# Kernel tuning notes

Hardware: AMD Instinct MI355X
Metric: run time of the kernel (lower is better)

Reference implementation:

```python
import jax, jax.numpy as jnp
import numpy as np
from jax import lax

B, C, H, W = 64, 512, 14, 14
HEAD_DIM = 32
NUM_HEADS = C // HEAD_DIM
HIDDEN = int(C * 4.0)
EPS = 1e-5
LS_INIT = 1e-5


def setup_inputs() -> dict:
    key = jax.random.key(0)
    ks = jax.random.split(key, 16)
    d = {}
    d['x'] = jax.random.normal(ks[0], (B, C, H, W), dtype=jnp.float32)
    # shared BatchNorm2d(dim) (inference-mode, running stats)
    d['bn_g'] = 1.0 + 0.1 * jax.random.normal(ks[1], (C,), dtype=jnp.float32)
    d['bn_b'] = 0.1 * jax.random.normal(ks[2], (C,), dtype=jnp.float32)
    d['bn_m'] = 0.1 * jax.random.normal(ks[3], (C,), dtype=jnp.float32)
    d['bn_v'] = jax.random.uniform(ks[4], (C,), minval=0.5, maxval=1.5, dtype=jnp.float32)
    # MHSA params (qkv_bias=False)
    d['qkv_w'] = 0.02 * jax.random.normal(ks[5], (3 * C, C), dtype=jnp.float32)
    d['proj_w'] = 0.02 * jax.random.normal(ks[6], (C, C), dtype=jnp.float32)
    d['proj_b'] = jnp.zeros((C,), dtype=jnp.float32)
    # ConvFFN: depthwise 7x7 (groups=C, no bias) -> BN -> 1x1 -> GELU -> 1x1
    d['dw_w'] = 0.02 * jax.random.normal(ks[7], (C, 1, 7, 7), dtype=jnp.float32)
    d['fbn_g'] = 1.0 + 0.1 * jax.random.normal(ks[8], (C,), dtype=jnp.float32)
    d['fbn_b'] = 0.1 * jax.random.normal(ks[9], (C,), dtype=jnp.float32)
    d['fbn_m'] = 0.1 * jax.random.normal(ks[10], (C,), dtype=jnp.float32)
    d['fbn_v'] = jax.random.uniform(ks[11], (C,), minval=0.5, maxval=1.5, dtype=jnp.float32)
    d['fc1_w'] = 0.02 * jax.random.normal(ks[12], (HIDDEN, C), dtype=jnp.float32)
    d['fc1_b'] = jnp.zeros((HIDDEN,), dtype=jnp.float32)
    d['fc2_w'] = 0.02 * jax.random.normal(ks[13], (C, HIDDEN), dtype=jnp.float32)
    d['fc2_b'] = jnp.zeros((C,), dtype=jnp.float32)
    # layer scale params, shape (C,1,1)
    d['ls1'] = LS_INIT * jnp.ones((C, 1, 1), dtype=jnp.float32)
    d['ls2'] = LS_INIT * jnp.ones((C, 1, 1), dtype=jnp.float32)
    return d


def _bn2d(x, g, b, m, v):
    # inference BatchNorm2d over channel dim of NCHW
    inv = g * lax.rsqrt(v + EPS)
    return x * inv[None, :, None, None] + (b - m * inv)[None, :, None, None]


def _mhsa(x, qkv_w, proj_w, proj_b):
    b, c, h, w = x.shape
    n = h * w
    xt = x.reshape(b, c, n).transpose(0, 2, 1)              # [B,N,C]
    qkv = xt @ qkv_w.T                                       # [B,N,3C]
    qkv = qkv.reshape(b, n, 3, NUM_HEADS, HEAD_DIM).transpose(2, 0, 3, 1, 4)
    q, k, v = qkv[0], qkv[1], qkv[2]                         # [B,h,N,d]
    scale = HEAD_DIM ** -0.5
    attn = jax.nn.softmax(jnp.einsum('bhnd,bhmd->bhnm', q * scale, k), axis=-1)
    o = jnp.einsum('bhnm,bhmd->bhnd', attn, v)               # [B,h,N,d]
    o = o.transpose(0, 2, 1, 3).reshape(b, n, c)             # [B,N,C]
    o = o @ proj_w.T + proj_b
    return o.transpose(0, 2, 1).reshape(b, c, h, w)


def _convffn(x, dw_w, fbn_g, fbn_b, fbn_m, fbn_v, fc1_w, fc1_b, fc2_w, fc2_b):
    y = lax.conv_general_dilated(x, dw_w, window_strides=(1, 1),
                                 padding=[(3, 3), (3, 3)],
                                 feature_group_count=C,
                                 dimension_numbers=('NCHW', 'OIHW', 'NCHW'))
    y = _bn2d(y, fbn_g, fbn_b, fbn_m, fbn_v)
    y = jnp.einsum('bchw,oc->bohw', y, fc1_w) + fc1_b[None, :, None, None]
    y = jax.nn.gelu(y, approximate=False)
    y = jnp.einsum('bchw,oc->bohw', y, fc2_w) + fc2_b[None, :, None, None]
    return y


def reference(x, bn_g, bn_b, bn_m, bn_v, qkv_w, proj_w, proj_b,
              dw_w, fbn_g, fbn_b, fbn_m, fbn_v, fc1_w, fc1_b, fc2_w, fc2_b,
              ls1, ls2):
    xn = _bn2d(x, bn_g, bn_b, bn_m, bn_v)
    x = x + ls1[None] * _mhsa(xn, qkv_w, proj_w, proj_b)
    xn = _bn2d(x, bn_g, bn_b, bn_m, bn_v)
    x = x + ls2[None] * _convffn(xn, dw_w, fbn_g, fbn_b, fbn_m, fbn_v,
                                 fc1_w, fc1_b, fc2_w, fc2_b)
    return x
```

## Files before the change

kernel.cpp:

```cpp
#include <hip/hip_runtime.h>
#include <hip/hip_bf16.h>
#include <hip/hip_fp8.h>
#include <stdint.h>

#define NTOK 196
#define NB   64
#define CCH  512
#define HID  2048
#define MTOT (NB * NTOK)

typedef __attribute__((ext_vector_type(8))) short  short8v;
typedef __attribute__((ext_vector_type(4))) float  float4v;
typedef __attribute__((ext_vector_type(2))) int    int2v;


__device__ __forceinline__ void mfma_fp8(float4v& d, int2v a, int2v b) {
  asm("v_mfma_f32_16x16x32_fp8_fp8 %0, %1, %2, %0" : "+v"(d) : "v"(a), "v"(b));
}

__device__ __forceinline__ void gload_lds16(const void* gsrc, void* ldst) {
  __builtin_amdgcn_global_load_lds(
      (const __attribute__((address_space(1))) unsigned int*)gsrc,
      (__attribute__((address_space(3))) unsigned int*)ldst, 16, 0, 0);
}

__device__ __forceinline__ int swz4(int r) { return (r ^ (r >> 2)) & 3; }

__device__ __forceinline__ uint32_t cvt2_fp8(float a, float b) {
  uint32_t d;
  asm("v_cvt_pk_fp8_f32 %0, %1, %2" : "=v"(d) : "v"(a), "v"(b));
  return d;
}


__global__ void prep_consts(const float* __restrict__ bn_g, const float* __restrict__ bn_b,
                            const float* __restrict__ bn_m, const float* __restrict__ bn_v,
                            const float* __restrict__ fbn_g, const float* __restrict__ fbn_b,
                            const float* __restrict__ fbn_m, const float* __restrict__ fbn_v,
                            float* __restrict__ cst) {
  int c = blockIdx.x * blockDim.x + threadIdx.x;
  if (c < CCH) {
    float i1 = bn_g[c] * rsqrtf(bn_v[c] + 1e-5f);
    cst[c] = i1;
    cst[512 + c] = bn_b[c] - bn_m[c] * i1;
    float i2 = fbn_g[c] * rsqrtf(fbn_v[c] + 1e-5f);
    cst[1024 + c] = i2;
    cst[1536 + c] = fbn_b[c] - fbn_m[c] * i2;
  }
}


__global__ void cvt_weights(const float* __restrict__ qkv_w, const float* __restrict__ proj_w,
                            const float* __restrict__ fc1_w, const float* __restrict__ fc2_w,
                            uint8_t* __restrict__ qkvb, uint8_t* __restrict__ projb,
                            uint8_t* __restrict__ fc1b, uint8_t* __restrict__ fc2b) {
  int i4 = blockIdx.x * blockDim.x + threadIdx.x;
  const int nq = 1536 * 512 / 4;
  const int np = 512 * 512 / 4;
  const int n1 = 2048 * 512 / 4;
  const float* src;
  uint8_t* dst;
  int k;
  if (i4 < nq)                { src = qkv_w;  dst = qkvb;  k = i4; }
  else if (i4 < nq + np)      { src = proj_w; dst = projb; k = i4 - nq; }
  else if (i4 < nq + np + n1) { src = fc1_w;  dst = fc1b;  k = i4 - nq - np; }
  else                        { src = fc2_w;  dst = fc2b;  k = i4 - nq - np - n1; }
  float4v v = *(const float4v*)(src + 4 * (size_t)k);
  uint32_t w0 = cvt2_fp8(v[0] * 16.0f, v[1] * 16.0f);
  uint32_t w1 = cvt2_fp8(v[2] * 16.0f, v[3] * 16.0f);
  *(uint16_t*)(dst + 4 * (size_t)k)     = (uint16_t)w0;
  *(uint16_t*)(dst + 4 * (size_t)k + 2) = (uint16_t)w1;
}


__global__ __launch_bounds__(256) void transpose_x(
    const float* __restrict__ x, uint8_t* __restrict__ xnt8,
    __hip_bfloat16* __restrict__ xt, const float* __restrict__ cst) {
  __shared__ float tile[32][33];
  const int n0 = blockIdx.x * 32;
  const int c0 = blockIdx.y * 32;
  const int b  = blockIdx.z;
  const int j = threadIdx.x & 31, i = threadIdx.x >> 5;
  #pragma unroll
  for (int p = 0; p < 4; ++p) {
    int cc = c0 + i + p * 8;
    int n = n0 + j;
    if (n < NTOK) tile[i + p * 8][j] = x[((size_t)b * CCH + cc) * NTOK + n];
  }
  __syncthreads();
  const float s = cst[c0 + j], t = cst[512 + c0 + j];
  float bn[4];
  size_t off[4];
  bool ok[4];
  #pragma unroll
  for (int p = 0; p < 4; ++p) {
    int n = n0 + i + p * 8;
    int cc = c0 + j;
    ok[p] = (n < NTOK);
    if (ok[p]) {
      float raw = tile[j][i + p * 8];
      size_t o = ((size_t)b * NTOK + n) * CCH + cc;
      xt[o] = __float2bfloat16(raw);
      bn[p] = raw * s + t;
      off[p] = o;
    }
  }
  uint32_t w0 = cvt2_fp8(bn[0], bn[1]);
  uint32_t w1 = cvt2_fp8(bn[2], bn[3]);
  if (ok[0]) xnt8[off[0]] = (uint8_t)w0;
  if (ok[1]) xnt8[off[1]] = (uint8_t)(w0 >> 8);
  if (ok[2]) xnt8[off[2]] = (uint8_t)w1;
  if (ok[3]) xnt8[off[3]] = (uint8_t)(w1 >> 8);
}


template<int EPI>
__global__ __launch_bounds__(256, 3) void gemm8f(
    const uint8_t* __restrict__ A, const uint8_t* __restrict__ Bw,
    int N, int K, int NY,
    __hip_bfloat16* __restrict__ outb, uint8_t* __restrict__ out8,
    float* __restrict__ outf,
    const float* __restrict__ bias, const float* __restrict__ ls,
    const __hip_bfloat16* __restrict__ resid) {
  __shared__ char lds[49152];
  const int tid  = threadIdx.x;
  const int lane = tid & 63;
  const int wave = tid >> 6;

  const int q    = (int)gridDim.x >> 3;
  const int orig = blockIdx.x;
  const int wgid = (orig & 7) * q + (orig >> 3);
  const int bx = wgid / NY;
  const int by = wgid - bx * NY;

  const int m0 = bx * 128;
  const int n0 = by * 128;
  const int wm = (wave >> 1) * 64;
  const int wn = (wave & 1) * 64;
  const int KT = K >> 6;

  float4v acc[4][4] = {};

  auto stage = [&](int buf, int kt) {
    const int kb = kt * 64;
    char* base = lds + buf * 16384;
    #pragma unroll
    for (int i = 0; i < 2; ++i) {
      int L = i * 4096 + tid * 16;
      int row = L >> 6;
      int lc = ((L >> 4) & 3) ^ swz4(row);
      gload_lds16(A + (size_t)(m0 + row) * K + kb + lc * 16, base + L);
    }
    #pragma unroll
    for (int i = 0; i < 2; ++i) {
      int L = i * 4096 + tid * 16;
      int row = L >> 6;
      int lc = ((L >> 4) & 3) ^ swz4(row);
      gload_lds16(Bw + (size_t)(n0 + row) * K + kb + lc * 16, base + 8192 + L);
    }
  };

  auto compute = [&](int buf) {
    const char* bA = lds + buf * 16384;
    const char* bB = bA + 8192;
    const int g = lane >> 4;
    #pragma unroll
    for (int t = 0; t < 2; ++t) {
      int2v av[4], bv[4];
      #pragma unroll
      for (int f = 0; f < 4; ++f) {
        int row = wm + f * 16 + (lane & 15);
        int c16 = ((t << 1) | (g >> 1)) ^ swz4(row);
        av[f] = *(const int2v*)(bA + row * 64 + c16 * 16 + (g & 1) * 8);
      }
      #pragma unroll
      for (int j = 0; j < 4; ++j) {
        int row = wn + j * 16 + (lane & 15);
        int c16 = ((t << 1) | (g >> 1)) ^ swz4(row);
        bv[j] = *(const int2v*)(bB + row * 64 + c16 * 16 + (g & 1) * 8);
      }
      #pragma unroll
      for (int i = 0; i < 4; ++i)
        #pragma unroll
        for (int j = 0; j < 4; ++j)
          mfma_fp8(acc[i][j], av[i], bv[j]);
    }
  };

  stage(0, 0);
  stage(1, 1);
  int cur = 0;
  for (int kt = 0; kt < KT - 1; ++kt) {
    asm volatile("s_waitcnt vmcnt(4)" ::: "memory");
    __builtin_amdgcn_s_barrier();
    __builtin_amdgcn_sched_barrier(0);
    if (kt + 2 < KT) {
      int s = cur + 2; if (s >= 3) s -= 3;
      stage(s, kt + 2);
    }
    compute(cur);
    ++cur; if (cur == 3) cur = 0;
  }
  asm volatile("s_waitcnt vmcnt(0)" ::: "memory");
  __builtin_amdgcn_s_barrier();
  __builtin_amdgcn_sched_barrier(0);
  compute(cur);
  asm volatile("s_nop 7\n\ts_nop 7");

  const float RS = 0.0625f;

  if (EPI == 0) {
    #pragma unroll
    for (int i = 0; i < 4; ++i)
      #pragma unroll
      for (int j = 0; j < 4; ++j)
        #pragma unroll
        for (int r = 0; r < 4; r += 2) {
          int m = m0 + wm + i * 16 + ((lane >> 4) << 2) + r;
          int n = n0 + wn + j * 16 + (lane & 15);
          int bb = m / NTOK, tok = m - bb * NTOK;
          int bb2 = (m + 1) / NTOK, tok2 = (m + 1) - bb2 * NTOK;
          int sel = n >> 9, hh = (n >> 5) & 15, d = n & 31;
          uint32_t w = cvt2_fp8(acc[i][j][r] * RS, acc[i][j][r + 1] * RS);
          out8[(((size_t)(sel * 16 + hh) * NB + bb) * NTOK + tok) * 32 + d]  = (uint8_t)w;
          out8[(((size_t)(sel * 16 + hh) * NB + bb2) * NTOK + tok2) * 32 + d] = (uint8_t)(w >> 8);
        }
  } else if (EPI == 2) {
    #pragma unroll
    for (int i = 0; i < 4; ++i)
      #pragma unroll
      for (int j = 0; j < 4; ++j)
        #pragma unroll
        for (int r = 0; r < 4; r += 2) {
          int m = m0 + wm + i * 16 + ((lane >> 4) << 2) + r;
          int n = n0 + wn + j * 16 + (lane & 15);
          float z0 = acc[i][j][r] * RS + bias[n];
          float z1 = acc[i][j][r + 1] * RS + bias[n];
          float g0 = z0 / (1.0f + __expf(-1.702f * z0));
          float g1 = z1 / (1.0f + __expf(-1.702f * z1));
          uint32_t w = cvt2_fp8(g0, g1);
          out8[(size_t)m * N + n]       = (uint8_t)w;
          out8[(size_t)(m + 1) * N + n] = (uint8_t)(w >> 8);
        }
  } else if (EPI == 1) {
    #pragma unroll
    for (int i = 0; i < 4; ++i)
      #pragma unroll
      for (int j = 0; j < 4; ++j)
        #pragma unroll
        for (int r = 0; r < 4; ++r) {
          int m = m0 + wm + i * 16 + ((lane >> 4) << 2) + r;
          int n = n0 + wn + j * 16 + (lane & 15);
          float v = acc[i][j][r] * RS + bias[n];
          v = __bfloat162float(resid[(size_t)m * CCH + n]) + ls[n] * v;
          outb[(size_t)m * CCH + n] = __float2bfloat16(v);
        }
  } else {
    float* LT = (float*)lds;
    #pragma unroll 1
    for (int hh = 0; hh < 2; ++hh) {
      __syncthreads();
      if ((wn >> 6) == hh) {
        #pragma unroll
        for (int i = 0; i < 4; ++i)
          #pragma unroll
          for (int j = 0; j < 4; ++j)
            #pragma unroll
            for (int r = 0; r < 4; ++r) {
              int ml = wm + i * 16 + ((lane >> 4) << 2) + r;
              int nl = j * 16 + (lane & 15);
              int n = n0 + wn + nl;
              float v = acc[i][j][r] * RS + bias[n];
              v = __bfloat162float(resid[(size_t)(m0 + ml) * CCH + n]) + ls[n] * v;
              LT[nl * 129 + ml] = v;
            }
      }
      __syncthreads();
      {
        int ml0 = lane << 1;
        int mg = m0 + ml0;
        int bb0 = mg / NTOK;
        int tt0 = mg - bb0 * NTOK;
        int bb1 = (mg + 1) / NTOK;
        int tt1 = (mg + 1) - bb1 * NTOK;
        size_t base0 = (size_t)bb0 * (CCH * NTOK) + tt0;
        size_t base1 = (size_t)bb1 * (CCH * NTOK) + tt1;
        #pragma unroll
        for (int u = 0; u < 16; ++u) {
          int cr = wave * 16 + u;
          int cg = n0 + hh * 64 + cr;
          float v0 = LT[cr * 129 + ml0];
          float v1 = LT[cr * 129 + ml0 + 1];
          outf[base0 + (size_t)cg * NTOK] = v0;
          outf[base1 + (size_t)cg * NTOK] = v1;
        }
      }
    }
  }
}


__global__ __launch_bounds__(256, 3) void attn_kernel(
    const uint8_t* __restrict__ qkv8, uint8_t* __restrict__ o_t8) {
  __shared__ char sQ[208 * 48];
  __shared__ char sK[224 * 48];
  __shared__ char sV[32 * 240];
  __shared__ char sP[4][16 * 232];
  const int tid  = threadIdx.x;
  const int lane = tid & 63;
  const int wave = tid >> 6;
  const int b = blockIdx.x >> 4;
  const int h = blockIdx.x & 15;
  const size_t CHB = 6272;
  const uint8_t* Qg = qkv8 + ((size_t)(0 * 16 + h) * NB + b) * CHB;
  const uint8_t* Kg = qkv8 + ((size_t)(1 * 16 + h) * NB + b) * CHB;
  const uint8_t* Vg = qkv8 + ((size_t)(2 * 16 + h) * NB + b) * CHB;

  for (int i = tid; i < 144; i += 256) {
    int r = i / 12, w = i % 12;
    ((uint32_t*)(sQ + (196 + r) * 48))[w] = 0u;
  }
  for (int i = tid; i < 336; i += 256) {
    int r = i / 12, w = i % 12;
    ((uint32_t*)(sK + (196 + r) * 48))[w] = 0u;
  }
  for (int i = tid; i < 352; i += 256) {
    int d = i / 11, w = i % 11;
    ((uint32_t*)(sV + d * 240 + 196))[w] = 0u;
  }

  for (int c = tid; c < 392; c += 256) {
    int row = c >> 1, hf = c & 1;
    uint4 vq = *(const uint4*)(Qg + c * 16);
    *(uint4*)(sQ + row * 48 + hf * 16) = vq;
    uint4 vk = *(const uint4*)(Kg + c * 16);
    *(uint4*)(sK + row * 48 + hf * 16) = vk;
  }
  for (int u = tid; u < 784; u += 256) {
    int row = u >> 2, d0 = (u & 3) * 8;
    uint64_t w = *(const uint64_t*)(Vg + (size_t)u * 8);
    #pragma unroll
    for (int e = 0; e < 8; ++e)
      sV[(d0 + e) * 240 + row] = (char)(w >> (8 * e));
  }
  __syncthreads();

  const float scale = 0.17677669529663687f;
  char* Pw = sP[wave];
  const int g = lane >> 4;

  for (int mt = wave; mt < 13; mt += 4) {
    int qrow = mt * 16 + (lane & 15);
    int2v aq = *(const int2v*)(sQ + qrow * 48 + g * 8);

    float4v s[14];
    #pragma unroll
    for (int nt = 0; nt < 14; ++nt) {
      int krow = nt * 16 + (lane & 15);
      int2v bk = *(const int2v*)(sK + krow * 48 + g * 8);
      s[nt] = float4v{0.f, 0.f, 0.f, 0.f};
      mfma_fp8(s[nt], aq, bk);
    }
    asm volatile("s_nop 7\n\ts_nop 7");

    float mx[4] = {-INFINITY, -INFINITY, -INFINITY, -INFINITY};
    #pragma unroll
    for (int nt = 0; nt < 14; ++nt) {
      bool valid = (nt * 16 + (lane & 15)) < NTOK;
      #pragma unroll
      for (int r = 0; r < 4; ++r) {
        float v = valid ? s[nt][r] * scale : -INFINITY;
        s[nt][r] = v;
        mx[r] = fmaxf(mx[r], v);
      }
    }
    #pragma unroll
    for (int off = 1; off < 16; off <<= 1) {
      #pragma unroll
      for (int r = 0; r < 4; ++r) mx[r] = fmaxf(mx[r], __shfl_xor(mx[r], off));
    }
    float sum[4] = {0.f, 0.f, 0.f, 0.f};
    #pragma unroll
    for (int nt = 0; nt < 14; ++nt) {
      #pragma unroll
      for (int r = 0; r < 4; ++r) {
        float e = __expf(s[nt][r] - mx[r]);
        s[nt][r] = e;
        sum[r] += e;
      }
    }
    #pragma unroll
    for (int off = 1; off < 16; off <<= 1) {
      #pragma unroll
      for (int r = 0; r < 4; ++r) sum[r] += __shfl_xor(sum[r], off);
    }
    float rs[4];
    #pragma unroll
    for (int r = 0; r < 4; ++r) rs[r] = 1.0f / sum[r];

    #pragma unroll
    for (int nt = 0; nt < 14; ++nt) {
      int col = nt * 16 + (lane & 15);
      #pragma unroll
      for (int r = 0; r < 4; r += 2) {
        int prow = ((lane >> 4) << 2) + r;
        uint32_t w = cvt2_fp8(s[nt][r], s[nt][r + 1]);
        *(uint8_t*)(Pw + prow * 232 + col)       = (uint8_t)w;
        *(uint8_t*)(Pw + (prow + 1) * 232 + col) = (uint8_t)(w >> 8);
      }
    }

    float4v o0 = float4v{0.f, 0.f, 0.f, 0.f};
    float4v o1 = float4v{0.f, 0.f, 0.f, 0.f};
    #pragma unroll
    for (int ks = 0; ks < 7; ++ks) {
      int2v pa = *(const int2v*)(Pw + (lane & 15) * 232 + ks * 32 + g * 8);
      int2v v0 = *(const int2v*)(sV + (lane & 15) * 240 + ks * 32 + g * 8);
      int2v v1 = *(const int2v*)(sV + (16 + (lane & 15)) * 240 + ks * 32 + g * 8);
      mfma_fp8(o0, pa, v0);
      mfma_fp8(o1, pa, v1);
    }
    asm volatile("s_nop 7\n\ts_nop 7");

    #pragma unroll
    for (int r = 0; r < 4; ++r) {
      int trow = mt * 16 + ((lane >> 4) << 2) + r;
      if (trow < NTOK) {
        size_t ob = ((size_t)b * NTOK + trow) * CCH + h * 32 + (lane & 15);
        uint32_t w = cvt2_fp8(o0[r] * rs[r], o1[r] * rs[r]);
        o_t8[ob]      = (uint8_t)w;
        o_t8[ob + 16] = (uint8_t)(w >> 8);
      }
    }
  }
}


__global__ __launch_bounds__(448) void dwconv_tm(
    const __hip_bfloat16* __restrict__ x1t, const float* __restrict__ dw_w,
    const float* __restrict__ cst, uint8_t* __restrict__ yt8) {
  __shared__ float img[196][32];
  __shared__ float wgt[49][32];
  const int tid = threadIdx.x;
  const int b  = blockIdx.x >> 4;
  const int cb = (blockIdx.x & 15) * 32;
  const int c  = tid & 31;
  const int gc = cb + c;
  const float s = cst[gc], t0 = cst[512 + gc];
  #pragma unroll
  for (int k = 0; k < 14; ++k) {
    int p = (tid >> 5) + k * 14;
    img[p][c] = __bfloat162float(x1t[((size_t)b * NTOK + p) * CCH + gc]) * s + t0;
  }
  for (int i = tid; i < 49 * 32; i += 448) {
    int tap = i >> 5, cc = i & 31;
    wgt[tap][cc] = dw_w[(cb + cc) * 49 + tap];
  }
  __syncthreads();

  const int px = tid >> 5;
  float out[14];
  #pragma unroll
  for (int i = 0; i < 14; ++i) out[i] = 0.f;
  #pragma unroll 1
  for (int row = 0; row < 14; ++row) {
    float v[7];
    #pragma unroll
    for (int dx = 0; dx < 7; ++dx) {
      int ix = px + dx - 3;
      v[dx] = ((unsigned)ix < 14u) ? img[row * 14 + ix][c] : 0.f;
    }
    #pragma unroll
    for (int kk = 0; kk < 7; ++kk) {
      int py = row + 3 - kk;
      if (py >= 0 && py < 14) {
        float hsum = 0.f;
        #pragma unroll
        for (int dx = 0; dx < 7; ++dx) hsum = fmaf(v[dx], wgt[kk * 7 + dx][c], hsum);
        out[py] += hsum;
      }
    }
  }
  const float fs = cst[1024 + gc], ft = cst[1536 + gc];
  #pragma unroll
  for (int py = 0; py < 14; py += 2) {
    uint32_t w = cvt2_fp8(out[py] * fs + ft, out[py + 1] * fs + ft);
    yt8[((size_t)b * NTOK + py * 14 + px) * CCH + gc]       = (uint8_t)w;
    yt8[((size_t)b * NTOK + (py + 1) * 14 + px) * CCH + gc] = (uint8_t)(w >> 8);
  }
}


extern "C" void kernel_launch(void* const* d_in, const int* in_sizes, int n_in,
                              void* d_out, int out_size, void* d_ws, size_t ws_size,
                              hipStream_t stream) {
  const float* x      = (const float*)d_in[0];
  const float* bn_g   = (const float*)d_in[1];
  const float* bn_b   = (const float*)d_in[2];
  const float* bn_m   = (const float*)d_in[3];
  const float* bn_v   = (const float*)d_in[4];
  const float* qkv_w  = (const float*)d_in[5];
  const float* proj_w = (const float*)d_in[6];
  const float* proj_b = (const float*)d_in[7];
  const float* dw_w   = (const float*)d_in[8];
  const float* fbn_g  = (const float*)d_in[9];
  const float* fbn_b  = (const float*)d_in[10];
  const float* fbn_m  = (const float*)d_in[11];
  const float* fbn_v  = (const float*)d_in[12];
  const float* fc1_w  = (const float*)d_in[13];
  const float* fc1_b  = (const float*)d_in[14];
  const float* fc2_w  = (const float*)d_in[15];
  const float* fc2_b  = (const float*)d_in[16];
  const float* ls1    = (const float*)d_in[17];
  const float* ls2    = (const float*)d_in[18];

  char* ws = (char*)d_ws;
  float* cst             = (float*)ws;
  uint8_t* qkvb8         = (uint8_t*)(ws + 32768);
  uint8_t* projb8        = (uint8_t*)(ws + 819200);
  uint8_t* fc1b8         = (uint8_t*)(ws + 1081344);
  uint8_t* fc2b8         = (uint8_t*)(ws + 2129920);
  uint8_t* xnt8          = (uint8_t*)(ws + 3178496);
  __hip_bfloat16* xt     = (__hip_bfloat16*)(ws + 9601024);
  uint8_t* qkv8          = (uint8_t*)(ws + 22446080);
  uint8_t* ot8           = (uint8_t*)(ws + 60981248);
  __hip_bfloat16* x1t    = (__hip_bfloat16*)(ws + 67403776);
  uint8_t* yt8           = (uint8_t*)(ws + 80248832);
  uint8_t* h8            = (uint8_t*)(ws + 3178496);

  prep_consts<<<dim3(2), dim3(256), 0, stream>>>(bn_g, bn_b, bn_m, bn_v,
                                                 fbn_g, fbn_b, fbn_m, fbn_v, cst);
  cvt_weights<<<dim3(3072), dim3(256), 0, stream>>>(qkv_w, proj_w, fc1_w, fc2_w,
                                                    qkvb8, projb8, fc1b8, fc2b8);
  transpose_x<<<dim3(7, 16, 64), dim3(256), 0, stream>>>(x, xnt8, xt, cst);
  gemm8f<0><<<dim3(1176), dim3(256), 0, stream>>>(xnt8, qkvb8, 1536, 512, 12,
                                                  nullptr, qkv8, nullptr, nullptr, nullptr, nullptr);
  attn_kernel<<<dim3(1024), dim3(256), 0, stream>>>(qkv8, ot8);
  gemm8f<1><<<dim3(392), dim3(256), 0, stream>>>(ot8, projb8, 512, 512, 4,
                                                 x1t, nullptr, nullptr, proj_b, ls1, xt);
  dwconv_tm<<<dim3(1024), dim3(448), 0, stream>>>(x1t, dw_w, cst, yt8);
  gemm8f<2><<<dim3(1568), dim3(256), 0, stream>>>(yt8, fc1b8, 2048, 512, 16,
                                                  nullptr, h8, nullptr, fc1_b, nullptr, nullptr);
  gemm8f<3><<<dim3(392), dim3(256), 0, stream>>>(h8, fc2b8, 512, 2048, 4,
                                                 nullptr, nullptr, (float*)d_out, fc2_b, ls2, x1t);
}
```

Measured before the change: 195.2 us.

## Replace triple-buffered K pipeline with single-stage 512-wide K chunk loads

The FP8 GEMM drops the 3-stage LDS ring of 64-wide K tiles and instead loads a full 512-wide K chunk of A and B (128 KB of LDS) in one stage, then runs all MFMAs from LDS. The swizzle changes to XOR over 32 sixteen-byte columns. The goal is fewer barriers and waitcnt points per tile, and whole-K residency for the K=512 GEMMs. In exchange occupancy falls to one block per CU, and global loads no longer overlap with compute inside a block, so latency hiding has to come from other CUs or blocks.

```diff
diff --git a/kernel.cpp b/kernel.cpp
--- a/kernel.cpp
+++ b/kernel.cpp
@@ -115,17 +115,19 @@
 
 
 template<int EPI>
-__global__ __launch_bounds__(256, 3) void gemm8f(
+__global__ __launch_bounds__(256, 1) void gemm1s(
     const uint8_t* __restrict__ A, const uint8_t* __restrict__ Bw,
     int N, int K, int NY,
     __hip_bfloat16* __restrict__ outb, uint8_t* __restrict__ out8,
     float* __restrict__ outf,
     const float* __restrict__ bias, const float* __restrict__ ls,
     const __hip_bfloat16* __restrict__ resid) {
-  __shared__ char lds[49152];
+  __shared__ char lds[131072];
   const int tid  = threadIdx.x;
   const int lane = tid & 63;
   const int wave = tid >> 6;
+  const int g    = lane >> 4;
+  const int l15  = lane & 15;
 
   const int q    = (int)gridDim.x >> 3;
   const int orig = blockIdx.x;
@@ -137,47 +139,50 @@
   const int n0 = by * 128;
   const int wm = (wave >> 1) * 64;
   const int wn = (wave & 1) * 64;
-  const int KT = K >> 6;
+  const int KCH = K >> 9;
 
   float4v acc[4][4] = {};
 
-  auto stage = [&](int buf, int kt) {
-    const int kb = kt * 64;
-    char* base = lds + buf * 16384;
-    #pragma unroll
-    for (int i = 0; i < 2; ++i) {
-      int L = i * 4096 + tid * 16;
-      int row = L >> 6;
-      int lc = ((L >> 4) & 3) ^ swz4(row);
-      gload_lds16(A + (size_t)(m0 + row) * K + kb + lc * 16, base + L);
-    }
-    #pragma unroll
-    for (int i = 0; i < 2; ++i) {
-      int L = i * 4096 + tid * 16;
-      int row = L >> 6;
-      int lc = ((L >> 4) & 3) ^ swz4(row);
-      gload_lds16(Bw + (size_t)(n0 + row) * K + kb + lc * 16, base + 8192 + L);
+  auto stageAB = [&](int ch) {
+    const int kb = ch << 9;
+    #pragma unroll
+    for (int u = 0; u < 16; ++u) {
+      int L = u * 4096 + tid * 16;
+      int r = L >> 9;
+      int pc = (L >> 4) & 31;
+      int lc = pc ^ (r & 31);
+      gload_lds16(A + (size_t)(m0 + r) * K + kb + lc * 16, lds + L);
+    }
+    #pragma unroll
+    for (int u = 0; u < 16; ++u) {
+      int L = u * 4096 + tid * 16;
+      int r = L >> 9;
+      int pc = (L >> 4) & 31;
+      int lc = pc ^ (r & 31);
+      gload_lds16(Bw + (size_t)(n0 + r) * K + kb + lc * 16, lds + 65536 + L);
     }
   };
 
-  auto compute = [&](int buf) {
-    const char* bA = lds + buf * 16384;
-    const char* bB = bA + 8192;
-    const int g = lane >> 4;
-    #pragma unroll
-    for (int t = 0; t < 2; ++t) {
+  #pragma unroll 1
+  for (int ch = 0; ch < KCH; ++ch) {
+    if (ch) __syncthreads();
+    stageAB(ch);
+    __syncthreads();
+    #pragma unroll
+    for (int kt = 0; kt < 16; ++kt) {
+      const int c16 = kt * 2 + (g >> 1);
       int2v av[4], bv[4];
       #pragma unroll
       for (int f = 0; f < 4; ++f) {
-        int row = wm + f * 16 + (lane & 15);
-        int c16 = ((t << 1) | (g >> 1)) ^ swz4(row);
-        av[f] = *(const int2v*)(bA + row * 64 + c16 * 16 + (g & 1) * 8);
+        int r = wm + f * 16 + l15;
+        int pc = c16 ^ (r & 31);
+        av[f] = *(const int2v*)(lds + r * 512 + pc * 16 + (g & 1) * 8);
       }
       #pragma unroll
       for (int j = 0; j < 4; ++j) {
-        int row = wn + j * 16 + (lane & 15);
-        int c16 = ((t << 1) | (g >> 1)) ^ swz4(row);
-        bv[j] = *(const int2v*)(bB + row * 64 + c16 * 16 + (g & 1) * 8);
+        int r = wn + j * 16 + l15;
+        int pc = c16 ^ (r & 31);
+        bv[j] = *(const int2v*)(lds + 65536 + r * 512 + pc * 16 + (g & 1) * 8);
       }
       #pragma unroll
       for (int i = 0; i < 4; ++i)
@@ -185,26 +190,7 @@
         for (int j = 0; j < 4; ++j)
           mfma_fp8(acc[i][j], av[i], bv[j]);
     }
-  };
-
-  stage(0, 0);
-  stage(1, 1);
-  int cur = 0;
-  for (int kt = 0; kt < KT - 1; ++kt) {
-    asm volatile("s_waitcnt vmcnt(4)" ::: "memory");
-    __builtin_amdgcn_s_barrier();
-    __builtin_amdgcn_sched_barrier(0);
-    if (kt + 2 < KT) {
-      int s = cur + 2; if (s >= 3) s -= 3;
-      stage(s, kt + 2);
-    }
-    compute(cur);
-    ++cur; if (cur == 3) cur = 0;
-  }
-  asm volatile("s_waitcnt vmcnt(0)" ::: "memory");
-  __builtin_amdgcn_s_barrier();
-  __builtin_amdgcn_sched_barrier(0);
-  compute(cur);
+  }
   asm volatile("s_nop 7\n\ts_nop 7");
 
   const float RS = 0.0625f;
@@ -216,8 +202,8 @@
       for (int j = 0; j < 4; ++j)
         #pragma unroll
         for (int r = 0; r < 4; r += 2) {
-          int m = m0 + wm + i * 16 + ((lane >> 4) << 2) + r;
-          int n = n0 + wn + j * 16 + (lane & 15);
+          int m = m0 + wm + i * 16 + (g << 2) + r;
+          int n = n0 + wn + j * 16 + l15;
           int bb = m / NTOK, tok = m - bb * NTOK;
           int bb2 = (m + 1) / NTOK, tok2 = (m + 1) - bb2 * NTOK;
           int sel = n >> 9, hh = (n >> 5) & 15, d = n & 31;
@@ -232,8 +218,8 @@
       for (int j = 0; j < 4; ++j)
         #pragma unroll
         for (int r = 0; r < 4; r += 2) {
-          int m = m0 + wm + i * 16 + ((lane >> 4) << 2) + r;
-          int n = n0 + wn + j * 16 + (lane & 15);
+          int m = m0 + wm + i * 16 + (g << 2) + r;
+          int n = n0 + wn + j * 16 + l15;
           float z0 = acc[i][j][r] * RS + bias[n];
           float z1 = acc[i][j][r + 1] * RS + bias[n];
           float g0 = z0 / (1.0f + __expf(-1.702f * z0));
@@ -249,8 +235,8 @@
       for (int j = 0; j < 4; ++j)
         #pragma unroll
         for (int r = 0; r < 4; ++r) {
-          int m = m0 + wm + i * 16 + ((lane >> 4) << 2) + r;
-          int n = n0 + wn + j * 16 + (lane & 15);
+          int m = m0 + wm + i * 16 + (g << 2) + r;
+          int n = n0 + wn + j * 16 + l15;
           float v = acc[i][j][r] * RS + bias[n];
           v = __bfloat162float(resid[(size_t)m * CCH + n]) + ls[n] * v;
           outb[(size_t)m * CCH + n] = __float2bfloat16(v);
@@ -267,8 +253,8 @@
           for (int j = 0; j < 4; ++j)
             #pragma unroll
             for (int r = 0; r < 4; ++r) {
-              int ml = wm + i * 16 + ((lane >> 4) << 2) + r;
-              int nl = j * 16 + (lane & 15);
+              int ml = wm + i * 16 + (g << 2) + r;
+              int nl = j * 16 + l15;
               int n = n0 + wn + nl;
               float v = acc[i][j][r] * RS + bias[n];
               v = __bfloat162float(resid[(size_t)(m0 + ml) * CCH + n]) + ls[n] * v;
@@ -533,14 +519,14 @@
   cvt_weights<<<dim3(3072), dim3(256), 0, stream>>>(qkv_w, proj_w, fc1_w, fc2_w,
                                                     qkvb8, projb8, fc1b8, fc2b8);
   transpose_x<<<dim3(7, 16, 64), dim3(256), 0, stream>>>(x, xnt8, xt, cst);
-  gemm8f<0><<<dim3(1176), dim3(256), 0, stream>>>(xnt8, qkvb8, 1536, 512, 12,
+  gemm1s<0><<<dim3(1176), dim3(256), 0, stream>>>(xnt8, qkvb8, 1536, 512, 12,
                                                   nullptr, qkv8, nullptr, nullptr, nullptr, nullptr);
   attn_kernel<<<dim3(1024), dim3(256), 0, stream>>>(qkv8, ot8);
-  gemm8f<1><<<dim3(392), dim3(256), 0, stream>>>(ot8, projb8, 512, 512, 4,
+  gemm1s<1><<<dim3(392), dim3(256), 0, stream>>>(ot8, projb8, 512, 512, 4,
                                                  x1t, nullptr, nullptr, proj_b, ls1, xt);
   dwconv_tm<<<dim3(1024), dim3(448), 0, stream>>>(x1t, dw_w, cst, yt8);
-  gemm8f<2><<<dim3(1568), dim3(256), 0, stream>>>(yt8, fc1b8, 2048, 512, 16,
+  gemm1s<2><<<dim3(1568), dim3(256), 0, stream>>>(yt8, fc1b8, 2048, 512, 16,
                                                   nullptr, h8, nullptr, fc1_b, nullptr, nullptr);
-  gemm8f<3><<<dim3(392), dim3(256), 0, stream>>>(h8, fc2b8, 512, 2048, 4,
+  gemm1s<3><<<dim3(392), dim3(256), 0, stream>>>(h8, fc2b8, 512, 2048, 4,
                                                  nullptr, nullptr, (float*)d_out, fc2_b, ls2, x1t);
 }
```

Result: slower. 252.6 us (+29.4%).
